# Performance work log

Hardware: AMD Instinct MI355X
Metric: run time of the kernel (lower is better)

The kernel has to match this reference:

```python
import jax, jax.numpy as jnp
import numpy as np
jax.config.update("jax_enable_x64", True)

N = 16384   # nodes
C = 16      # initial color vocabulary size
B = 64      # number of graphs in the batch
_rs = np.random.RandomState(42)
_MULTS = jnp.asarray((_rs.randint(1, 2 ** 62, size=C + 1).astype(np.int64) << 1) | 1)  # odd 64-bit hash multipliers


def setup_inputs() -> dict:
    key = jax.random.key(0)
    k1, k2, k3 = jax.random.split(key, 3)
    x = jax.random.randint(k1, (N,), 0, C, dtype=jnp.int64)
    adj_t = jax.random.randint(k2, (N, N), 0, 2).astype(jnp.float32)  # dense binary adjacency
    batch = jnp.sort(jax.random.randint(k3, (N,), 0, B, dtype=jnp.int64))
    return {"x": x, "adj_t": adj_t, "batch": batch}


def _wl_colors(x, adj_t):
    # One WL refinement step. The torch code hashes (own_color, sorted neighbor colors)
    # and assigns new ids by insertion order into an OrderedDict ('isolate' -> 0).
    # A sorted tuple of neighbor colors is equivalent to the neighbor color multiset,
    # which we represent as a count histogram and hash with a 64-bit wraparound
    # polynomial hash; ids are then assigned by first-occurrence (node-index) order.
    n = x.shape[0]
    onehot = jax.nn.one_hot(x, C, dtype=adj_t.dtype)                 # [N, C]
    nbr_hist = jnp.round(adj_t @ onehot).astype(jnp.int64)           # [N, C] neighbor color counts
    iso = (adj_t.sum(axis=1) + adj_t.sum(axis=0)) == 0               # isolated nodes
    h = x * _MULTS[0] + (nbr_hist * _MULTS[1:]).sum(axis=-1)         # int64 wraparound hash
    h = jnp.where(iso, jnp.int64(-(2 ** 63)), h)
    order = jnp.argsort(h)
    hs = h[order]
    new_grp = jnp.concatenate([jnp.ones((1,), bool), hs[1:] != hs[:-1]])
    gid = jnp.zeros(n, jnp.int64).at[order].set(jnp.cumsum(new_grp) - 1)   # group id per node
    first_of_grp = jax.ops.segment_min(jnp.arange(n), gid, num_segments=n)
    firsts = first_of_grp[gid]                                       # first node index with same signature
    is_first = (~iso) & (firsts == jnp.arange(n))
    rank = jnp.cumsum(is_first.astype(jnp.int64))                    # hashmap insertion order (1-based)
    return jnp.where(iso, 0, rank[firsts])                           # 'isolate' -> 0


def _histogram(colors, batch):
    # Per-graph color histogram; width padded to N+1 (max possible distinct colors)
    # for static shapes -- extra columns are zero and do not affect the L2 norm.
    num_colors = N + 1
    idx = batch * num_colors + colors
    out = jnp.zeros(B * num_colors, jnp.int64).at[idx].add(1)
    out = out.reshape(B, num_colors)[:, 1:]                          # drop 'isolate' column
    out = out.astype(jnp.float64)
    return out / jnp.linalg.norm(out, axis=-1, keepdims=True)


def reference(x, adj_t, batch):
    colors = _wl_colors(x, adj_t)          # forward's default return value
    hist = _histogram(colors, batch)       # return_embedding=True output
    return hist, colors
```

## Files before the change

kernel.cpp:

```cpp
#include <hip/hip_runtime.h>
#include <stdint.h>

#define NN 16384
#define NC 16
#define NB 64

typedef unsigned int vuint4 __attribute__((ext_vector_type(4)));

struct Mults { unsigned long long m[17]; };


__global__ __launch_bounds__(256) void k_init(const int* __restrict__ x,
                                              unsigned long long* __restrict__ table,
                                              int* __restrict__ scount,
                                              int* __restrict__ cnt) {
  int idx = blockIdx.x * 256 + threadIdx.x;
  if (idx == 0) *scount = 0;
  if (idx < 4096) {
    int c = idx & 15, k = (idx >> 4) & 3, chunk = idx >> 6;
    unsigned long long m = 0ull;
    for (int l = 0; l < 64; ++l) {
      int col = chunk * 256 + l * 4 + k;
      if (x[col] == c) m |= (1ull << l);
    }
    table[idx] = m;
  }
  int4 z = {0, 0, 0, 0};
  int4* c4 = (int4*)cnt;
  #pragma unroll
  for (int r = 0; r < 4; ++r) c4[(size_t)idx * 4 + r] = z;
}

__global__ __launch_bounds__(256) void k_hist(const float* __restrict__ adj,
                                              const unsigned long long* __restrict__ table,
                                              const int* __restrict__ x,
                                              Mults M,
                                              unsigned long long* __restrict__ h,
                                              int* __restrict__ iso,
                                              int* __restrict__ firsts,
                                              int* __restrict__ suspects,
                                              int* __restrict__ scount) {
  int wave = threadIdx.x >> 6;
  int lane = threadIdx.x & 63;
  int row  = blockIdx.x * 4 + wave;
  int xv   = x[row];
  const vuint4* rowp = (const vuint4*)(adj + (size_t)row * NN);
  int c = lane & 15, k = lane >> 6 ? 0 : (lane >> 4);
  k = lane >> 4;
  const unsigned long long* tk = table + (k * 16 + c);
  int cnt = 0;
  #pragma unroll 4
  for (int chunk = 0; chunk < 64; ++chunk) {
    vuint4 v = __builtin_nontemporal_load(&rowp[chunk * 64 + lane]);
    unsigned long long tm = tk[chunk * 64];
    unsigned long long b0 = __ballot(v.x != 0u);
    unsigned long long b1 = __ballot(v.y != 0u);
    unsigned long long b2 = __ballot(v.z != 0u);
    unsigned long long b3 = __ballot(v.w != 0u);
    unsigned long long m = (k & 2) ? ((k & 1) ? b3 : b2) : ((k & 1) ? b1 : b0);
    cnt += __popcll(m & tm);
  }
  cnt += __shfl_xor(cnt, 16, 64);
  cnt += __shfl_xor(cnt, 32, 64);
  int rs = cnt;
  rs += __shfl_xor(rs, 1, 64);
  rs += __shfl_xor(rs, 2, 64);
  rs += __shfl_xor(rs, 4, 64);
  rs += __shfl_xor(rs, 8, 64);
  unsigned long long hl = (unsigned long long)(long long)cnt * M.m[(lane & 15) + 1];
  hl += __shfl_xor(hl, 1, 64);
  hl += __shfl_xor(hl, 2, 64);
  hl += __shfl_xor(hl, 4, 64);
  hl += __shfl_xor(hl, 8, 64);
  if (lane == 0) {
    h[row] = hl + (unsigned long long)(long long)xv * M.m[0];
    if (rs == 0) { int s = atomicAdd(scount, 1); suspects[s] = row; }
  }
  if (lane == 1) iso[row] = 0;
  if (lane == 2) firsts[row] = 0x7fffffff;
}

__global__ __launch_bounds__(256) void k_colcheck(const float* __restrict__ adj,
                                                  const int* __restrict__ suspects,
                                                  const int* __restrict__ scount,
                                                  int* __restrict__ iso,
                                                  unsigned long long* __restrict__ h) {
  __shared__ int red[256];
  int nsus = *scount;
  for (int u = blockIdx.x; u < nsus; u += gridDim.x) {
    int col = suspects[u];
    int any = 0;
    for (int r = threadIdx.x; r < NN; r += 256)
      any |= (adj[(size_t)r * NN + col] != 0.0f);
    red[threadIdx.x] = any;
    __syncthreads();
    for (int s = 128; s > 0; s >>= 1) {
      if (threadIdx.x < s) red[threadIdx.x] |= red[threadIdx.x + s];
      __syncthreads();
    }
    if (threadIdx.x == 0 && red[0] == 0) {
      iso[col] = 1;
      h[col] = 0x8000000000000000ull;
    }
    __syncthreads();
  }
}

#define JC 2048
__global__ __launch_bounds__(256) void k_firsts(const unsigned long long* __restrict__ h,
                                                int* __restrict__ firsts) {
  __shared__ unsigned long long hs[JC];
  int jbase = blockIdx.y * JC;
  for (int t = threadIdx.x; t < JC; t += 256) hs[t] = h[jbase + t];
  __syncthreads();
  int i = blockIdx.x * 256 + threadIdx.x;
  unsigned long long hi = h[i];
  int best = 0x7fffffff;
  #pragma unroll 8
  for (int jj = 0; jj < JC; ++jj) {
    if (hs[jj] == hi) best = min(best, jbase + jj);
  }
  if (best < 0x7fffffff) atomicMin(&firsts[i], best);
}

__global__ __launch_bounds__(1024) void k_scan(const int* __restrict__ iso,
                                               const int* __restrict__ firsts,
                                               const int* __restrict__ batch,
                                               float* __restrict__ out_colors,
                                               int* __restrict__ cnt) {
  __shared__ int rank_lds[NN];
  __shared__ int wsum[16];
  int t = threadIdx.x;
  int lane = t & 63, wv = t >> 6;
  int base = t * 16;
  int loc[16];
  int s = 0;
  #pragma unroll
  for (int u = 0; u < 16; ++u) {
    int i = base + u;
    int isf = (!iso[i]) && (firsts[i] == i);
    s += isf;
    loc[u] = s;
  }
  int incl = s;
  #pragma unroll
  for (int off = 1; off < 64; off <<= 1) {
    int v = __shfl_up(incl, off, 64);
    if (lane >= off) incl += v;
  }
  if (lane == 63) wsum[wv] = incl;
  __syncthreads();
  if (t == 0) {
    int acc = 0;
    #pragma unroll
    for (int w = 0; w < 16; ++w) { int v = wsum[w]; wsum[w] = acc; acc += v; }
  }
  __syncthreads();
  int excl = wsum[wv] + incl - s;
  #pragma unroll
  for (int u = 0; u < 16; ++u) rank_lds[base + u] = excl + loc[u];
  __syncthreads();
  #pragma unroll
  for (int u = 0; u < 16; ++u) {
    int i = base + u;
    int c = iso[i] ? 0 : rank_lds[firsts[i]];
    out_colors[i] = (float)c;
    if (c > 0) atomicAdd(&cnt[(size_t)batch[i] * NN + (c - 1)], 1);
  }
}

__global__ __launch_bounds__(256) void k_norm(const int* __restrict__ cnt,
                                              float* __restrict__ out) {
  __shared__ float red[256];
  int b = blockIdx.x;
  const int4* c4 = (const int4*)(cnt + (size_t)b * NN);
  float4* o4 = (float4*)(out + (size_t)b * NN);
  float ss = 0.0f;
  for (int j = threadIdx.x; j < NN / 4; j += 256) {
    int4 v = c4[j];
    float4 f = {(float)v.x, (float)v.y, (float)v.z, (float)v.w};
    ss += f.x * f.x + f.y * f.y + f.z * f.z + f.w * f.w;
  }
  red[threadIdx.x] = ss;
  __syncthreads();
  for (int s = 128; s > 0; s >>= 1) {
    if (threadIdx.x < s) red[threadIdx.x] += red[threadIdx.x + s];
    __syncthreads();
  }
  float inv = 1.0f / sqrtf(red[0]);
  for (int j = threadIdx.x; j < NN / 4; j += 256) {
    int4 v = c4[j];
    float4 f = {(float)v.x * inv, (float)v.y * inv, (float)v.z * inv, (float)v.w * inv};
    o4[j] = f;
  }
}


struct MTState { uint32_t mt[624]; int idx; };

static void mt_seed(MTState& s, uint32_t seed) {
  s.mt[0] = seed;
  for (int i = 1; i < 624; ++i)
    s.mt[i] = 1812433253u * (s.mt[i - 1] ^ (s.mt[i - 1] >> 30)) + (uint32_t)i;
  s.idx = 624;
}

static uint32_t mt_next(MTState& s) {
  if (s.idx >= 624) {
    for (int i = 0; i < 624; ++i) {
      uint32_t y = (s.mt[i] & 0x80000000u) | (s.mt[(i + 1) % 624] & 0x7fffffffu);
      uint32_t nx = s.mt[(i + 397) % 624] ^ (y >> 1);
      if (y & 1u) nx ^= 2567483615u;
      s.mt[i] = nx;
    }
    s.idx = 0;
  }
  uint32_t y = s.mt[s.idx++];
  y ^= y >> 11;
  y ^= (y << 7) & 2636928640u;
  y ^= (y << 15) & 4022730752u;
  y ^= y >> 18;
  return y;
}

static uint64_t mt_next64(MTState& s) {
  uint64_t hi = mt_next(s);
  uint64_t lo = mt_next(s);
  return (hi << 32) | lo;
}


extern "C" void kernel_launch(void* const* d_in, const int* in_sizes, int n_in,
                              void* d_out, int out_size, void* d_ws, size_t ws_size,
                              hipStream_t stream) {
  const int*   x     = (const int*)d_in[0];
  const float* adj   = (const float*)d_in[1];
  const int*   batch = (const int*)d_in[2];
  float* out_hist   = (float*)d_out;
  float* out_colors = out_hist + (size_t)NB * NN;

  char* ws = (char*)d_ws;
  int*                cnt      = (int*)(ws + 0);
  int*                scount   = (int*)(ws + 4194304);
  int*                suspects = (int*)(ws + 4194560);
  unsigned long long* h        = (unsigned long long*)(ws + 4260096);
  int*                iso      = (int*)(ws + 4391168);
  int*                firsts   = (int*)(ws + 4456704);
  unsigned long long* table    = (unsigned long long*)(ws + 4522240);

  Mults M;
  {
    MTState st;
    mt_seed(st, 42u);
    const uint64_t mask62 = (1ull << 62) - 1ull;
    const uint64_t rng    = (1ull << 62) - 2ull;
    for (int i = 0; i < 17; ++i) {
      uint64_t v;
      do { v = mt_next64(st) & mask62; } while (v > rng);
      M.m[i] = ((1ull + v) << 1) | 1ull;
    }
  }

  k_init<<<256, 256, 0, stream>>>(x, table, scount, cnt);
  k_hist<<<NN / 4, 256, 0, stream>>>(adj, table, x, M, h, iso, firsts, suspects, scount);
  k_colcheck<<<64, 256, 0, stream>>>(adj, suspects, scount, iso, h);
  dim3 gf(NN / 256, NN / JC);
  k_firsts<<<gf, 256, 0, stream>>>(h, firsts);
  k_scan<<<1, 1024, 0, stream>>>(iso, firsts, batch, out_colors, cnt);
  k_norm<<<NB, 256, 0, stream>>>(cnt, out_hist);
}
```

Baseline: 1.402 ms.

## Replace quadratic first-occurrence search with global open-addressing hash table

Removes the all-pairs k_firsts kernel, which compared every node hash against every other node. Each node's hash is now inserted into a linear-probing global hash table with atomicCAS, and atomicMin on the value keeps the smallest row index. The scan kernel looks up each node's first occurrence in that table. This trades an O(N^2) comparison pass for atomics during hist and colcheck, plus dependent global-memory probes inside the single-block scan kernel, which may add latency.

```diff
diff --git a/kernel.cpp b/kernel.cpp
--- a/kernel.cpp
+++ b/kernel.cpp
@@ -4,16 +4,46 @@
 #define NN 16384
 #define NC 16
 #define NB 64
+#define HT 65536
+#define EMPTYK 0xFFFFFFFFFFFFFFFFull
 
 typedef unsigned int vuint4 __attribute__((ext_vector_type(4)));
 
 struct Mults { unsigned long long m[17]; };
+
+
+__device__ __forceinline__ uint32_t hslot(unsigned long long v) {
+  return (uint32_t)((v * 0x9E3779B97F4A7C15ull) >> 48) & (HT - 1);
+}
+
+__device__ __forceinline__ void ht_insert(unsigned long long* __restrict__ key,
+                                          int* __restrict__ val,
+                                          unsigned long long hval, int row) {
+  uint32_t s = hslot(hval);
+  while (true) {
+    unsigned long long old = atomicCAS(&key[s], EMPTYK, hval);
+    if (old == EMPTYK || old == hval) { atomicMin(&val[s], row); return; }
+    s = (s + 1) & (HT - 1);
+  }
+}
+
+__device__ __forceinline__ int ht_find(const unsigned long long* __restrict__ key,
+                                       const int* __restrict__ val,
+                                       unsigned long long hval) {
+  uint32_t s = hslot(hval);
+  while (true) {
+    if (key[s] == hval) return val[s];
+    s = (s + 1) & (HT - 1);
+  }
+}
 
 
 __global__ __launch_bounds__(256) void k_init(const int* __restrict__ x,
                                               unsigned long long* __restrict__ table,
                                               int* __restrict__ scount,
-                                              int* __restrict__ cnt) {
+                                              int* __restrict__ cnt,
+                                              unsigned long long* __restrict__ htkey,
+                                              int* __restrict__ htval) {
   int idx = blockIdx.x * 256 + threadIdx.x;
   if (idx == 0) *scount = 0;
   if (idx < 4096) {
@@ -25,6 +55,8 @@
     }
     table[idx] = m;
   }
+  htkey[idx] = EMPTYK;
+  htval[idx] = 0x7fffffff;
   int4 z = {0, 0, 0, 0};
   int4* c4 = (int4*)cnt;
   #pragma unroll
@@ -37,16 +69,16 @@
                                               Mults M,
                                               unsigned long long* __restrict__ h,
                                               int* __restrict__ iso,
-                                              int* __restrict__ firsts,
                                               int* __restrict__ suspects,
-                                              int* __restrict__ scount) {
+                                              int* __restrict__ scount,
+                                              unsigned long long* __restrict__ htkey,
+                                              int* __restrict__ htval) {
   int wave = threadIdx.x >> 6;
   int lane = threadIdx.x & 63;
   int row  = blockIdx.x * 4 + wave;
   int xv   = x[row];
   const vuint4* rowp = (const vuint4*)(adj + (size_t)row * NN);
-  int c = lane & 15, k = lane >> 6 ? 0 : (lane >> 4);
-  k = lane >> 4;
+  int c = lane & 15, k = lane >> 4;
   const unsigned long long* tk = table + (k * 16 + c);
   int cnt = 0;
   #pragma unroll 4
@@ -73,18 +105,21 @@
   hl += __shfl_xor(hl, 4, 64);
   hl += __shfl_xor(hl, 8, 64);
   if (lane == 0) {
-    h[row] = hl + (unsigned long long)(long long)xv * M.m[0];
+    unsigned long long hv = hl + (unsigned long long)(long long)xv * M.m[0];
+    h[row] = hv;
     if (rs == 0) { int s = atomicAdd(scount, 1); suspects[s] = row; }
+    else          ht_insert(htkey, htval, hv, row);
   }
   if (lane == 1) iso[row] = 0;
-  if (lane == 2) firsts[row] = 0x7fffffff;
 }
 
 __global__ __launch_bounds__(256) void k_colcheck(const float* __restrict__ adj,
                                                   const int* __restrict__ suspects,
                                                   const int* __restrict__ scount,
                                                   int* __restrict__ iso,
-                                                  unsigned long long* __restrict__ h) {
+                                                  unsigned long long* __restrict__ h,
+                                                  unsigned long long* __restrict__ htkey,
+                                                  int* __restrict__ htval) {
   __shared__ int red[256];
   int nsus = *scount;
   for (int u = blockIdx.x; u < nsus; u += gridDim.x) {
@@ -98,33 +133,23 @@
       if (threadIdx.x < s) red[threadIdx.x] |= red[threadIdx.x + s];
       __syncthreads();
     }
-    if (threadIdx.x == 0 && red[0] == 0) {
-      iso[col] = 1;
-      h[col] = 0x8000000000000000ull;
+    if (threadIdx.x == 0) {
+      unsigned long long hv = h[col];
+      if (red[0] == 0) {
+        hv = 0x8000000000000000ull;
+        iso[col] = 1;
+        h[col] = hv;
+      }
+      ht_insert(htkey, htval, hv, col);
     }
     __syncthreads();
   }
 }
 
-#define JC 2048
-__global__ __launch_bounds__(256) void k_firsts(const unsigned long long* __restrict__ h,
-                                                int* __restrict__ firsts) {
-  __shared__ unsigned long long hs[JC];
-  int jbase = blockIdx.y * JC;
-  for (int t = threadIdx.x; t < JC; t += 256) hs[t] = h[jbase + t];
-  __syncthreads();
-  int i = blockIdx.x * 256 + threadIdx.x;
-  unsigned long long hi = h[i];
-  int best = 0x7fffffff;
-  #pragma unroll 8
-  for (int jj = 0; jj < JC; ++jj) {
-    if (hs[jj] == hi) best = min(best, jbase + jj);
-  }
-  if (best < 0x7fffffff) atomicMin(&firsts[i], best);
-}
-
 __global__ __launch_bounds__(1024) void k_scan(const int* __restrict__ iso,
-                                               const int* __restrict__ firsts,
+                                               const unsigned long long* __restrict__ h,
+                                               const unsigned long long* __restrict__ htkey,
+                                               const int* __restrict__ htval,
                                                const int* __restrict__ batch,
                                                float* __restrict__ out_colors,
                                                int* __restrict__ cnt) {
@@ -134,11 +159,15 @@
   int lane = t & 63, wv = t >> 6;
   int base = t * 16;
   int loc[16];
+  int fl[16];
   int s = 0;
   #pragma unroll
   for (int u = 0; u < 16; ++u) {
     int i = base + u;
-    int isf = (!iso[i]) && (firsts[i] == i);
+    int f = ht_find(htkey, htval, h[i]);
+    int is_iso = iso[i];
+    fl[u] = is_iso ? -1 : f;
+    int isf = (!is_iso) && (f == i);
     s += isf;
     loc[u] = s;
   }
@@ -163,7 +192,7 @@
   #pragma unroll
   for (int u = 0; u < 16; ++u) {
     int i = base + u;
-    int c = iso[i] ? 0 : rank_lds[firsts[i]];
+    int c = (fl[u] < 0) ? 0 : rank_lds[fl[u]];
     out_colors[i] = (float)c;
     if (c > 0) atomicAdd(&cnt[(size_t)batch[i] * NN + (c - 1)], 1);
   }
@@ -245,8 +274,9 @@
   int*                suspects = (int*)(ws + 4194560);
   unsigned long long* h        = (unsigned long long*)(ws + 4260096);
   int*                iso      = (int*)(ws + 4391168);
-  int*                firsts   = (int*)(ws + 4456704);
-  unsigned long long* table    = (unsigned long long*)(ws + 4522240);
+  unsigned long long* table    = (unsigned long long*)(ws + 4456704);
+  unsigned long long* htkey    = (unsigned long long*)(ws + 4489472);
+  int*                htval    = (int*)(ws + 5013760);
 
   Mults M;
   {
@@ -261,11 +291,9 @@
     }
   }
 
-  k_init<<<256, 256, 0, stream>>>(x, table, scount, cnt);
-  k_hist<<<NN / 4, 256, 0, stream>>>(adj, table, x, M, h, iso, firsts, suspects, scount);
-  k_colcheck<<<64, 256, 0, stream>>>(adj, suspects, scount, iso, h);
-  dim3 gf(NN / 256, NN / JC);
-  k_firsts<<<gf, 256, 0, stream>>>(h, firsts);
-  k_scan<<<1, 1024, 0, stream>>>(iso, firsts, batch, out_colors, cnt);
+  k_init<<<256, 256, 0, stream>>>(x, table, scount, cnt, htkey, htval);
+  k_hist<<<NN / 4, 256, 0, stream>>>(adj, table, x, M, h, iso, suspects, scount, htkey, htval);
+  k_colcheck<<<64, 256, 0, stream>>>(adj, suspects, scount, iso, h, htkey, htval);
+  k_scan<<<1, 1024, 0, stream>>>(iso, h, htkey, htval, batch, out_colors, cnt);
   k_norm<<<NB, 256, 0, stream>>>(cnt, out_hist);
 }
```

After: 1.403 ms. No clear change (+0.1%).
